# Kernel tuning notes

Hardware: AMD Instinct MI355X
Metric: run time of the kernel (lower is better)

The kernel has to match this reference:

```python
import jax, jax.numpy as jnp
import numpy as np

N = 16384
D_IN = 64
D_HID = D_IN // 2  # 32
D_OUT = 32


def setup_inputs() -> dict:
    key = jax.random.key(0)
    kA, kX, k1, k2, k3 = jax.random.split(key, 5)
    # Dense adjacency-like operator [N, N]; scaled so activations stay sane.
    A = jax.random.normal(kA, (N, N), dtype=jnp.float32) / np.sqrt(N)
    X = jax.random.normal(kX, (N, D_IN), dtype=jnp.float32)
    # torch nn.Linear weights: [out_features, in_features], no bias
    W1 = jax.random.normal(k1, (D_IN, D_IN), dtype=jnp.float32) / np.sqrt(D_IN)
    W2 = jax.random.normal(k2, (D_HID, D_IN), dtype=jnp.float32) / np.sqrt(D_IN)
    W3 = jax.random.normal(k3, (D_OUT, D_HID), dtype=jnp.float32) / np.sqrt(D_HID)
    return {"A": A, "X": X, "W1": W1, "W2": W2, "W3": W3}


def reference(A, X, W1, W2, W3):
    # Layer 1: relu(fc1(A @ X)); fc(x) = x @ W.T
    h = jax.nn.relu((A @ X) @ W1.T)        # [N, D_IN]
    # Layer 2: relu(fc2(A @ h))
    h = jax.nn.relu((A @ h) @ W2.T)        # [N, D_HID]
    # Layer 3: fc3(A @ h), no activation
    return (A @ h) @ W3.T                  # [N, D_OUT]
```

## Files before the change

### kernel.cpp

```cpp
#include <hip/hip_runtime.h>
#include <cstdint>
#include <cstddef>


#define NN 16384
#define SK1 8
#define KC1 (NN / SK1)
#define CH 512
#define NCH (KC1 / CH)
#define SK2 16
#define KC2 (NN / SK2)
#define NKB (NN / 32)

typedef __attribute__((ext_vector_type(8))) short s16x8;
typedef __attribute__((ext_vector_type(4))) float fx4;

__device__ __forceinline__ unsigned short f2bf_rne(float f) {
    unsigned int x = __builtin_bit_cast(unsigned int, f);
    x += 0x7fffu + ((x >> 16) & 1u);
    return (unsigned short)(x >> 16);
}

__device__ __forceinline__ s16x8 pack_bf(fx4 a, fx4 b) {
    s16x8 t;
    t[0] = (short)f2bf_rne(a[0]);
    t[1] = (short)f2bf_rne(a[1]);
    t[2] = (short)f2bf_rne(a[2]);
    t[3] = (short)f2bf_rne(a[3]);
    t[4] = (short)f2bf_rne(b[0]);
    t[5] = (short)f2bf_rne(b[1]);
    t[6] = (short)f2bf_rne(b[2]);
    t[7] = (short)f2bf_rne(b[3]);
    return t;
}

template <int SAVE>
__global__ __launch_bounds__(256, 4) void k_spmm1(
    const float* __restrict__ A32,
    unsigned short* __restrict__ Abf,
    const unsigned short* __restrict__ PT,
    float* __restrict__ part)
{
    __shared__ unsigned short Asm[2][16 * 512];
    const int tid  = threadIdx.x;
    const int lane = tid & 63, wv = tid >> 6;
    const int srow = lane & 15, kg = lane >> 4;
    const int s  = blockIdx.y;
    const int gR = blockIdx.x;
    const long R = (long)gR * 16;
    const long kbeg = (long)s * KC1;

    fx4 acc = (fx4){0.f, 0.f, 0.f, 0.f};
    fx4 gld[8];

    auto LOADG = [&](int c) {
#pragma unroll
        for (int j = 0; j < 8; ++j) {
            const int u = wv * 8 + j;
            const int r = u >> 1, seg = u & 1;
            const float* p = A32 + (R + r) * (long)NN + kbeg + (long)c * CH
                             + seg * 256 + lane * 4;
            gld[j] = __builtin_nontemporal_load((const fx4*)p);
        }
    };
    auto STORE_LDS = [&](int buf) {
#pragma unroll
        for (int j = 0; j < 8; ++j) {
            const int u = wv * 8 + j;
            const int r = u >> 1, seg = u & 1;
            const int kt = seg * 256 + lane * 4;
            const int kblk = kt >> 5;
            const int kb   = kt & 31;
            const int flane = (r & 15) + (((kb & 15) >> 2) << 4);
            const int half  = kb >> 4;
            uint2 v;
            v.x = (unsigned)f2bf_rne(gld[j][0]) | ((unsigned)f2bf_rne(gld[j][1]) << 16);
            v.y = (unsigned)f2bf_rne(gld[j][2]) | ((unsigned)f2bf_rne(gld[j][3]) << 16);
            const int boff = kblk * 1024 + ((flane * 16 + half * 8) ^ ((kblk & 7) << 4));
            *(uint2*)((char*)&Asm[buf][0] + boff) = v;
        }
    };
    auto COMPUTE = [&](int buf, int c) {
#pragma unroll
        for (int ks = 0; ks < 16; ++ks) {
            const int aoff = ks * 1024 + ((lane * 16) ^ ((ks & 7) << 4));
            s16x8 af = *(const s16x8*)((const char*)&Asm[buf][0] + aoff);
            s16x8 bf = *(const s16x8*)(PT + (long)(wv * 16 + srow) * NN + kbeg
                                       + (long)c * CH + ks * 32 + kg * 8);
            acc = __builtin_amdgcn_mfma_f32_16x16x32_bf16(af, bf, acc, 0, 0, 0);
        }
        if (SAVE) {
            const long kb0 = (kbeg + (long)c * CH) >> 5;
#pragma unroll
            for (int t = 0; t < 4; ++t) {
                const int kblk = wv * 4 + t;
                const int aoff = kblk * 1024 + ((lane * 16) ^ ((kblk & 7) << 4));
                s16x8 v = *(const s16x8*)((const char*)&Asm[buf][0] + aoff);
                *(s16x8*)(Abf + (((long)gR * NKB + kb0 + kblk) * 64 + lane) * 8) = v;
            }
        }
    };

    LOADG(0);
    STORE_LDS(0);
    __syncthreads();
    for (int c = 0; c < NCH; ++c) {
        if (c + 1 < NCH) LOADG(c + 1);
        COMPUTE(c & 1, c);
        if (c + 1 < NCH) STORE_LDS((c + 1) & 1);
        __syncthreads();
    }

    float* pb = part + (long)s * NN * 64 + R * 64;
#pragma unroll
    for (int r = 0; r < 4; ++r)
        pb[(kg * 4 + r) * 64 + wv * 16 + srow] = acc[r];
}

template <int ABF>
__global__ __launch_bounds__(256, 4) void k_spmm2(
    const unsigned short* __restrict__ Abf,
    const float* __restrict__ A32,
    const unsigned short* __restrict__ PT,
    float* __restrict__ part)
{
    const int lane = threadIdx.x & 63;
    const int wv   = threadIdx.x >> 6;
    const int srow = lane & 15;
    const int kg   = lane >> 4;
    const int s    = blockIdx.y;
    const long kbeg = (long)s * KC2;
    const int rowbase = blockIdx.x * 256 + wv * 64;
    const long g0 = rowbase >> 4;

    fx4 acc[4][2];
#pragma unroll
    for (int t = 0; t < 4; ++t)
#pragma unroll
        for (int c = 0; c < 2; ++c) acc[t][c] = (fx4){0.f, 0.f, 0.f, 0.f};

#pragma unroll 2
    for (int i = 0; i < KC2 / 32; ++i) {
        const long ko = kbeg + (long)i * 32;
        const long kblk = ko >> 5;
        s16x8 af[4];
        if (ABF) {
#pragma unroll
            for (int t = 0; t < 4; ++t)
                af[t] = *(const s16x8*)(Abf + (((g0 + t) * NKB + kblk) * 64 + lane) * 8);
        } else {
#pragma unroll
            for (int t = 0; t < 4; ++t) {
                const float* p = A32 + (long)(rowbase + t * 16 + srow) * NN + ko + kg * 4;
                fx4 a0 = __builtin_nontemporal_load((const fx4*)p);
                fx4 a1 = __builtin_nontemporal_load((const fx4*)(p + 16));
                af[t] = pack_bf(a0, a1);
            }
        }
        s16x8 b0 = *(const s16x8*)(PT + (long)srow * NN + ko + kg * 8);
        s16x8 b1 = *(const s16x8*)(PT + (long)(16 + srow) * NN + ko + kg * 8);
#pragma unroll
        for (int t = 0; t < 4; ++t) {
            acc[t][0] = __builtin_amdgcn_mfma_f32_16x16x32_bf16(af[t], b0, acc[t][0], 0, 0, 0);
            acc[t][1] = __builtin_amdgcn_mfma_f32_16x16x32_bf16(af[t], b1, acc[t][1], 0, 0, 0);
        }
    }
    float* pbase = part + (long)s * NN * 32;
#pragma unroll
    for (int t = 0; t < 4; ++t)
#pragma unroll
        for (int c = 0; c < 2; ++c)
#pragma unroll
            for (int r = 0; r < 4; ++r)
                pbase[(long)(rowbase + t * 16 + kg * 4 + r) * 32 + c * 16 + srow] = acc[t][c][r];
}

template <int DIN, int DOUT, int NSUM, bool RELU>
__global__ __launch_bounds__(256) void k_proj(
    const float* __restrict__ src,
    const float* __restrict__ W,
    unsigned short* __restrict__ PT)
{
    __shared__ float Ws[DOUT * DIN];
    __shared__ float Hs[64][DIN + 1];
    const int tid = threadIdx.x;
    for (int i = tid; i < DOUT * DIN; i += 256) Ws[i] = W[i];
    const int rbase = blockIdx.x * 64;
    for (int i = tid; i < 64 * DIN; i += 256) {
        const int rl = i / DIN, k = i % DIN;
        float v = 0.f;
#pragma unroll
        for (int s2 = 0; s2 < NSUM; ++s2)
            v += src[(long)s2 * NN * DIN + (long)(rbase + rl) * DIN + k];
        Hs[rl][k] = RELU ? fmaxf(v, 0.f) : v;
    }
    __syncthreads();
    const int rl = tid & 63;
    const int c0 = tid >> 6;
    const int r  = rbase + rl;
    const int kk = r & 31;
    const int pidx = (r & ~31) + ((kk & 15) >> 2) * 8 + (kk & 3) + ((kk >> 4) << 2);
    for (int c = c0; c < DOUT; c += 4) {
        float accv = 0.f;
#pragma unroll
        for (int k = 0; k < DIN; ++k) accv += Hs[rl][k] * Ws[c * DIN + k];
        PT[(long)c * NN + pidx] = f2bf_rne(accv);
    }
}

__global__ __launch_bounds__(256) void k_red(
    const float* __restrict__ part, float* __restrict__ out)
{
    const int e = blockIdx.x * 256 + threadIdx.x;
    if (e >= NN * 32 / 4) return;
    fx4 v = (fx4){0.f, 0.f, 0.f, 0.f};
#pragma unroll
    for (int s = 0; s < SK2; ++s)
        v += *(const fx4*)(part + (long)s * NN * 32 + (long)e * 4);
    *(fx4*)(out + (long)e * 4) = v;
}

extern "C" void kernel_launch(void* const* d_in, const int* in_sizes, int n_in,
                              void* d_out, int out_size, void* d_ws, size_t ws_size,
                              hipStream_t stream) {
    const float* A  = (const float*)d_in[0];
    const float* X  = (const float*)d_in[1];
    const float* W1 = (const float*)d_in[2];
    const float* W2 = (const float*)d_in[3];
    const float* W3 = (const float*)d_in[4];
    float* out = (float*)d_out;

    char* ws = (char*)d_ws;
    const size_t part_b = (size_t)SK1 * NN * 64 * 4;
    const size_t pt_b   = (size_t)64 * NN * 2;
    const size_t abf_b  = (size_t)NN * NN * 2;
    float*          part = (float*)ws;
    unsigned short* PT   = (unsigned short*)(ws + part_b);
    unsigned short* Abf  = (unsigned short*)(ws + part_b + pt_b);
    const bool save = ws_size >= part_b + pt_b + abf_b;

    dim3 b(256);
    dim3 gP(NN / 64);
    dim3 g1(NN / 16, SK1);
    dim3 g2(NN / 256, SK2);

    k_proj<64, 64, 1, false><<<gP, b, 0, stream>>>(X, W1, PT);
    if (save) k_spmm1<1><<<g1, b, 0, stream>>>(A, Abf, PT, part);
    else      k_spmm1<0><<<g1, b, 0, stream>>>(A, Abf, PT, part);

    k_proj<64, 32, SK1, true><<<gP, b, 0, stream>>>(part, W2, PT);
    if (save) k_spmm2<1><<<g2, b, 0, stream>>>(Abf, A, PT, part);
    else      k_spmm2<0><<<g2, b, 0, stream>>>(Abf, A, PT, part);

    k_proj<32, 32, SK2, true><<<gP, b, 0, stream>>>(part, W3, PT);
    if (save) k_spmm2<1><<<g2, b, 0, stream>>>(Abf, A, PT, part);
    else      k_spmm2<0><<<g2, b, 0, stream>>>(Abf, A, PT, part);

    k_red<<<dim3(NN * 32 / 4 / 256), b, 0, stream>>>(part, out);
}
```

Measured before the change: 699.9 us.

## Stage fp32 A tiles via direct global-to-LDS loads and convert at MFMA time

Replaces the register-staged load, bf16 convert and LDS store of A in the first SpMM kernel with asynchronous global_load_lds DMA of raw fp32 into a row-swizzled LDS buffer. The bf16 packing now happens when MFMA fragments are read, and the saved bf16 copy of A is written from those fragments. The chunk size is halved so the fp32 double buffer fits in LDS. This is meant to free VGPRs and let loads overlap compute, at the cost of twice the LDS traffic per element and reliance on the barrier waiting for the async loads.

```diff
diff --git a/kernel.cpp b/kernel.cpp
--- a/kernel.cpp
+++ b/kernel.cpp
@@ -6,7 +6,7 @@
 #define NN 16384
 #define SK1 8
 #define KC1 (NN / SK1)
-#define CH 512
+#define CH 256
 #define NCH (KC1 / CH)
 #define SK2 16
 #define KC2 (NN / SK2)
@@ -34,6 +34,12 @@
     return t;
 }
 
+__device__ __forceinline__ void gload_lds16(const float* g, float* l) {
+    __builtin_amdgcn_global_load_lds(
+        (const __attribute__((address_space(1))) void*)g,
+        (__attribute__((address_space(3))) void*)l, 16, 0, 0);
+}
+
 template <int SAVE>
 __global__ __launch_bounds__(256, 4) void k_spmm1(
     const float* __restrict__ A32,
@@ -41,7 +47,7 @@
     const unsigned short* __restrict__ PT,
     float* __restrict__ part)
 {
-    __shared__ unsigned short Asm[2][16 * 512];
+    __shared__ float Asm[2][16 * CH];
     const int tid  = threadIdx.x;
     const int lane = tid & 63, wv = tid >> 6;
     const int srow = lane & 15, kg = lane >> 4;
@@ -51,63 +57,39 @@
     const long kbeg = (long)s * KC1;
 
     fx4 acc = (fx4){0.f, 0.f, 0.f, 0.f};
-    fx4 gld[8];
-
-    auto LOADG = [&](int c) {
-#pragma unroll
-        for (int j = 0; j < 8; ++j) {
-            const int u = wv * 8 + j;
-            const int r = u >> 1, seg = u & 1;
-            const float* p = A32 + (R + r) * (long)NN + kbeg + (long)c * CH
-                             + seg * 256 + lane * 4;
-            gld[j] = __builtin_nontemporal_load((const fx4*)p);
-        }
-    };
-    auto STORE_LDS = [&](int buf) {
-#pragma unroll
-        for (int j = 0; j < 8; ++j) {
-            const int u = wv * 8 + j;
-            const int r = u >> 1, seg = u & 1;
-            const int kt = seg * 256 + lane * 4;
-            const int kblk = kt >> 5;
-            const int kb   = kt & 31;
-            const int flane = (r & 15) + (((kb & 15) >> 2) << 4);
-            const int half  = kb >> 4;
-            uint2 v;
-            v.x = (unsigned)f2bf_rne(gld[j][0]) | ((unsigned)f2bf_rne(gld[j][1]) << 16);
-            v.y = (unsigned)f2bf_rne(gld[j][2]) | ((unsigned)f2bf_rne(gld[j][3]) << 16);
-            const int boff = kblk * 1024 + ((flane * 16 + half * 8) ^ ((kblk & 7) << 4));
-            *(uint2*)((char*)&Asm[buf][0] + boff) = v;
+
+    auto STAGE = [&](int buf, int c) {
+#pragma unroll
+        for (int j = 0; j < 4; ++j) {
+            const int r = wv * 4 + j;
+            const int sl = lane ^ (r & 7);
+            const float* g = A32 + (R + r) * (long)NN + kbeg + (long)c * CH + sl * 4;
+            gload_lds16(g, &Asm[buf][r * CH]);
         }
     };
     auto COMPUTE = [&](int buf, int c) {
-#pragma unroll
-        for (int ks = 0; ks < 16; ++ks) {
-            const int aoff = ks * 1024 + ((lane * 16) ^ ((ks & 7) << 4));
-            s16x8 af = *(const s16x8*)((const char*)&Asm[buf][0] + aoff);
+        const long kb0 = (kbeg + (long)c * CH) >> 5;
+        const float* rowp = &Asm[buf][srow * CH];
+#pragma unroll
+        for (int ks = 0; ks < CH / 32; ++ks) {
+            const int s0 = ((ks * 8 + kg) ^ (srow & 7)) * 4;
+            const int s1 = ((ks * 8 + 4 + kg) ^ (srow & 7)) * 4;
+            fx4 a0 = *(const fx4*)(rowp + s0);
+            fx4 a1 = *(const fx4*)(rowp + s1);
+            s16x8 af = pack_bf(a0, a1);
             s16x8 bf = *(const s16x8*)(PT + (long)(wv * 16 + srow) * NN + kbeg
                                        + (long)c * CH + ks * 32 + kg * 8);
             acc = __builtin_amdgcn_mfma_f32_16x16x32_bf16(af, bf, acc, 0, 0, 0);
-        }
-        if (SAVE) {
-            const long kb0 = (kbeg + (long)c * CH) >> 5;
-#pragma unroll
-            for (int t = 0; t < 4; ++t) {
-                const int kblk = wv * 4 + t;
-                const int aoff = kblk * 1024 + ((lane * 16) ^ ((kblk & 7) << 4));
-                s16x8 v = *(const s16x8*)((const char*)&Asm[buf][0] + aoff);
-                *(s16x8*)(Abf + (((long)gR * NKB + kb0 + kblk) * 64 + lane) * 8) = v;
-            }
+            if (SAVE && (ks >> 1) == wv)
+                *(s16x8*)(Abf + (((long)gR * NKB + kb0 + ks) * 64 + lane) * 8) = af;
         }
     };
 
-    LOADG(0);
-    STORE_LDS(0);
+    STAGE(0, 0);
     __syncthreads();
     for (int c = 0; c < NCH; ++c) {
-        if (c + 1 < NCH) LOADG(c + 1);
+        if (c + 1 < NCH) STAGE((c + 1) & 1, c + 1);
         COMPUTE(c & 1, c);
-        if (c + 1 < NCH) STORE_LDS((c + 1) & 1);
         __syncthreads();
     }
 
```

Result: no change. 694.5 us (-0.8%).
